# Performance work log

Hardware: AMD Instinct MI355X
Metric: run time of the kernel (lower is better)

## Reference

```python
import jax, jax.numpy as jnp
import numpy as np

B, QS, KS, E, H = 2, 2048, 2048, 2048, 16
D = E // H  # head_dim = 128
EPS = 1e-6


def setup_inputs() -> dict:
    key = jax.random.key(0)
    ks = jax.random.split(key, 11)
    scale_in = 1.0 / np.sqrt(E)  # lecun_normal fan_in = E
    scale_out = 1.0 / np.sqrt(E)  # fan_in for out proj = H*D = E
    return {
        "q": jax.random.normal(ks[0], (B, QS, E), jnp.float32),
        "kv": jax.random.normal(ks[1], (B, KS, E), jnp.float32),
        "q_pos": jax.random.normal(ks[2], (B, QS, E), jnp.float32),
        "kv_pos": jax.random.normal(ks[3], (B, KS, E), jnp.float32),
        "mask": jax.random.bernoulli(ks[4], 0.5, (B, QS, KS)),
        "wq": jax.random.normal(ks[5], (E, H, D), jnp.float32) * scale_in,
        "wk": jax.random.normal(ks[6], (E, H, D), jnp.float32) * scale_in,
        "wv": jax.random.normal(ks[7], (E, H, D), jnp.float32) * scale_in,
        "q_ln_scale": jnp.ones((D,), jnp.float32),
        "k_ln_scale": jnp.ones((D,), jnp.float32),
        "wo": jax.random.normal(ks[8], (H, D, E), jnp.float32) * scale_out,
    }


def _layernorm_no_bias(x, scale):
    # flax LayerNorm over last axis, use_bias=False, epsilon=1e-6
    mu = jnp.mean(x, axis=-1, keepdims=True)
    var = jnp.mean(jnp.square(x - mu), axis=-1, keepdims=True)
    return (x - mu) * jax.lax.rsqrt(var + EPS) * scale


def reference(q, kv, q_pos, kv_pos, mask, wq, wk, wv, q_ln_scale, k_ln_scale, wo):
    dtype = q.dtype
    qi = q + q_pos          # [b, qs, e]
    ki = kv + kv_pos        # [b, ks, e]
    vi = kv
    # QKV projections (DenseGeneral, no bias) -> [b, s, h, d]
    qh = jnp.einsum('bqe,ehd->bqhd', qi, wq)
    kh = jnp.einsum('bke,ehd->bkhd', ki, wk)
    vh = jnp.einsum('bke,ehd->bkhd', vi, wv)
    # normalize_qk: LayerNorm (no bias) on query/key over head_dim
    qh = _layernorm_no_bias(qh, q_ln_scale)
    kh = _layernorm_no_bias(kh, k_ln_scale)
    # scaled dot-product with float32 logits
    qh = qh / jnp.sqrt(jnp.asarray(D, dtype))
    logits = jnp.einsum('bqhd,bkhd->bhqk', qh, kh,
                        preferred_element_type=jnp.float32)
    big_neg = jnp.finfo(jnp.float32).min
    logits = jnp.where(mask[:, None, :, :], logits, big_neg)
    attn = jax.nn.softmax(logits, axis=-1).astype(dtype)  # [b,h,q,k]
    out = jnp.einsum('bhqk,bkhd->bqhd', attn, vh)
    # output projection (DenseGeneral over (h,d), no bias)
    return jnp.einsum('bqhd,hde->bqe', out, wo)
```

## Files before the change

### kernel.cpp

```cpp
#include <hip/hip_runtime.h>
#include <hip/hip_bf16.h>


typedef __attribute__((ext_vector_type(8))) __bf16 bf16x8;
typedef __attribute__((ext_vector_type(4))) float f32x4;
typedef __attribute__((ext_vector_type(16))) float f32x16;
typedef __attribute__((ext_vector_type(8))) unsigned short ushort8;
typedef __attribute__((ext_vector_type(4))) unsigned short ushort4v;
typedef __attribute__((ext_vector_type(4))) unsigned uint4v;
typedef __attribute__((ext_vector_type(4))) float float4v;

#define MFMA16(a, b, c) __builtin_amdgcn_mfma_f32_16x16x32_bf16((a), (b), (c), 0, 0, 0)
#define MFMA32(a, b, c) __builtin_amdgcn_mfma_f32_32x32x16_bf16((a), (b), (c), 0, 0, 0)

__device__ __forceinline__ unsigned short f2bf(float f) {
  unsigned u = __builtin_bit_cast(unsigned, f);
  u += 0x7fffu + ((u >> 16) & 1u);
  return (unsigned short)(u >> 16);
}

__device__ __forceinline__ unsigned pkbf(float lo, float hi) {
  unsigned d;
  asm("v_cvt_pk_bf16_f32 %0, %1, %2" : "=v"(d) : "v"(lo), "v"(hi));
  return d;
}

__device__ __forceinline__ float max3f(float a, float b, float c) {
  float d;
  asm("v_max3_f32 %0, %1, %2, %3" : "=v"(d) : "v"(a), "v"(b), "v"(c));
  return d;
}

__device__ __forceinline__ float exp2a(float x) {
  float d;
  asm("v_exp_f32 %0, %1" : "=v"(d) : "v"(x));
  return d;
}

__device__ __forceinline__ void gload_lds16(const void* g, void* l) {
  __builtin_amdgcn_global_load_lds(
      (const __attribute__((address_space(1))) void*)g,
      (__attribute__((address_space(3))) void*)l, 16, 0, 0);
}

__global__ __launch_bounds__(256) void k_prep(const float4v* __restrict__ q,
                                              const float4v* __restrict__ q_pos,
                                              const float4v* __restrict__ kv,
                                              const float4v* __restrict__ kv_pos,
                                              const int* __restrict__ mask,
                                              ushort4v* __restrict__ a_q,
                                              ushort4v* __restrict__ a_k,
                                              ushort4v* __restrict__ a_v,
                                              unsigned long long* __restrict__ mkb) {
  int bx = blockIdx.x, tid = threadIdx.x;
  if (bx < 8192) {
    int i = bx * 256 + tid;
    float4v a = q[i] + q_pos[i];
    ushort4v r;
    r[0] = f2bf(a[0]); r[1] = f2bf(a[1]); r[2] = f2bf(a[2]); r[3] = f2bf(a[3]);
    a_q[i] = r;
  } else if (bx < 16384) {
    int i = (bx - 8192) * 256 + tid;
    float4v a = kv[i];
    float4v s = a + kv_pos[i];
    ushort4v ra, rb;
    ra[0] = f2bf(s[0]); ra[1] = f2bf(s[1]); ra[2] = f2bf(s[2]); ra[3] = f2bf(s[3]);
    rb[0] = f2bf(a[0]); rb[1] = f2bf(a[1]); rb[2] = f2bf(a[2]); rb[3] = f2bf(a[3]);
    a_k[i] = ra; a_v[i] = rb;
  } else {
    int i = (bx - 16384) * 256 + tid;
    unsigned long long b = __ballot(mask[i] != 0);
    if ((tid & 63) == 0) mkb[i >> 6] = b;
  }
}

__global__ __launch_bounds__(256) void k_tr(const float* __restrict__ s0, const float* __restrict__ s1,
                                            const float* __restrict__ s2, const float* __restrict__ s3,
                                            unsigned short* __restrict__ d0, unsigned short* __restrict__ d1,
                                            unsigned short* __restrict__ d2, unsigned short* __restrict__ d3) {
  __shared__ float t[32][33];
  const float* S; unsigned short* D;
  switch (blockIdx.z) {
    case 0: S = s0; D = d0; break;
    case 1: S = s1; D = d1; break;
    case 2: S = s2; D = d2; break;
    default: S = s3; D = d3; break;
  }
  int x = threadIdx.x & 31, y = threadIdx.x >> 5;
  int r0 = blockIdx.y * 32, c0 = blockIdx.x * 32;
#pragma unroll
  for (int i = 0; i < 4; ++i) t[y + 8 * i][x] = S[(size_t)(r0 + y + 8 * i) * 2048 + c0 + x];
  __syncthreads();
#pragma unroll
  for (int i = 0; i < 4; ++i)
    D[(size_t)(c0 + y + 8 * i) * 2048 + r0 + x] = f2bf(t[x][y + 8 * i]);
}

template <int MODE>
__global__ __launch_bounds__(512, 2) void k_gemm8(const unsigned short* __restrict__ A,
                                                  const unsigned short* __restrict__ Bt,
                                                  void* __restrict__ Cv,
                                                  const float* __restrict__ lnsc) {
  constexpr int K = 2048;
  constexpr int NT = 32;
  constexpr int BUF = 49152;
  __shared__ __attribute__((aligned(16))) char smem[3 * BUF];
  int tid = threadIdx.x;
  int lane = tid & 63, w = tid >> 6;
  int wr = w >> 2, wc = w & 3;
  int r15 = lane & 15, blk = lane >> 4;
  int L = blockIdx.y * gridDim.x + blockIdx.x;
  int xcd = L & 7, slot = L >> 3;
  int mt, nt;
  if constexpr (MODE == 4) { mt = xcd; nt = slot; }
  else { mt = xcd * 2 + (slot >> 4); nt = slot & 15; }
  int n0 = nt * 128, m0 = mt * 256;
  const unsigned short* Abase = A + (size_t)m0 * K;
  const unsigned short* Bbase = Bt + (size_t)n0 * K;
  f32x4 acc[8][2] = {};

  const unsigned short* ag[4]; int al[4];
  const unsigned short* bg[2]; int bl[2];
#pragma unroll
  for (int i = 0; i < 4; ++i) {
    int c = i * 512 + tid;
    int row = c >> 3, cc = c & 7;
    ag[i] = Abase + (size_t)row * K + ((cc ^ (row & 7)) * 8);
    al[i] = c * 16;
  }
#pragma unroll
  for (int i = 0; i < 2; ++i) {
    int c = i * 512 + tid;
    int row = c >> 3, cc = c & 7;
    bg[i] = Bbase + (size_t)row * K + ((cc ^ (row & 7)) * 8);
    bl[i] = 32768 + c * 16;
  }

  auto stage = [&](int t) {
    char* buf = smem + (t % 3) * BUF;
    int kt = t * 64;
#pragma unroll
    for (int i = 0; i < 4; ++i) gload_lds16(ag[i] + kt, buf + al[i]);
#pragma unroll
    for (int i = 0; i < 2; ++i) gload_lds16(bg[i] + kt, buf + bl[i]);
  };

  stage(0);
  stage(1);

  for (int t = 0; t < NT; ++t) {
    if (t + 2 < NT) {
      stage(t + 2);
      asm volatile("s_waitcnt vmcnt(6)" ::: "memory");
    } else {
      asm volatile("s_waitcnt vmcnt(0)" ::: "memory");
    }
    __builtin_amdgcn_s_barrier();
    __builtin_amdgcn_sched_barrier(0);
    const unsigned short* sA = (const unsigned short*)(smem + (t % 3) * BUF);
    const unsigned short* sB = (const unsigned short*)(smem + (t % 3) * BUF + 32768);
#pragma unroll
    for (int kk = 0; kk < 2; ++kk) {
      bf16x8 av[8], bv[2];
#pragma unroll
      for (int i = 0; i < 8; ++i) {
        int row = wr * 128 + i * 16 + r15;
        av[i] = *(const bf16x8*)&sA[row * 64 + (((kk * 4 + blk) ^ (row & 7)) * 8)];
      }
#pragma unroll
      for (int j = 0; j < 2; ++j) {
        int row = wc * 32 + j * 16 + r15;
        bv[j] = *(const bf16x8*)&sB[row * 64 + (((kk * 4 + blk) ^ (row & 7)) * 8)];
      }
#pragma unroll
      for (int i = 0; i < 8; ++i)
#pragma unroll
        for (int j = 0; j < 2; ++j) acc[i][j] = MFMA16(av[i], bv[j], acc[i][j]);
    }
    asm volatile("s_waitcnt lgkmcnt(0)" ::: "memory");
    __builtin_amdgcn_s_barrier();
  }
  __syncthreads();

  if constexpr (MODE == 3) {
    float* C = (float*)Cv;
#pragma unroll
    for (int i = 0; i < 8; ++i)
#pragma unroll
      for (int r = 0; r < 4; ++r) {
        int rowl = wr * 128 + i * 16 + blk * 4 + r;
#pragma unroll
        for (int j = 0; j < 2; ++j) {
          int coll = wc * 32 + j * 16 + r15;
          C[(size_t)(m0 + rowl) * 2048 + n0 + coll] = acc[i][j][r];
        }
      }
  } else if constexpr (MODE == 4) {
    unsigned short* Vtp = (unsigned short*)Cv;
    int p15 = (r15 & 3) | ((r15 & 4) << 1) | ((r15 & 8) >> 1);
#pragma unroll
    for (int i = 0; i < 8; ++i)
#pragma unroll
      for (int r = 0; r < 4; ++r) {
        int rowg = m0 + wr * 128 + i * 16 + blk * 4 + r;
        int h = rowg >> 7, d = rowg & 127;
#pragma unroll
        for (int j = 0; j < 2; ++j) {
          int col = n0 + wc * 32 + j * 16;
          int b = col >> 11, s16 = col & 2047;
          Vtp[(((size_t)(b * 16 + h) * 128 + d) * 2048) + s16 + p15] = f2bf(acc[i][j][r]);
        }
      }
  } else {
    float* sSum = (float*)smem;
    float* sSq  = (float*)smem + 1024;
#pragma unroll
    for (int i = 0; i < 8; ++i)
#pragma unroll
      for (int r = 0; r < 4; ++r) {
        float v0 = acc[i][0][r], v1 = acc[i][1][r];
        float sm = v0 + v1, sq = v0 * v0 + v1 * v1;
        sm += __shfl_xor(sm, 1); sq += __shfl_xor(sq, 1);
        sm += __shfl_xor(sm, 2); sq += __shfl_xor(sq, 2);
        sm += __shfl_xor(sm, 4); sq += __shfl_xor(sq, 4);
        sm += __shfl_xor(sm, 8); sq += __shfl_xor(sq, 8);
        if (r15 == 0) {
          int rowl = wr * 128 + i * 16 + blk * 4 + r;
          sSum[wc * 256 + rowl] = sm;
          sSq[wc * 256 + rowl] = sq;
        }
      }
    __syncthreads();
    unsigned short* Hout = (unsigned short*)Cv;
    int h = nt;
#pragma unroll
    for (int i = 0; i < 8; ++i)
#pragma unroll
      for (int r = 0; r < 4; ++r) {
        int rowl = wr * 128 + i * 16 + blk * 4 + r;
        float sm = (sSum[rowl] + sSum[256 + rowl]) + (sSum[512 + rowl] + sSum[768 + rowl]);
        float sq = (sSq[rowl] + sSq[256 + rowl]) + (sSq[512 + rowl] + sSq[768 + rowl]);
        float mean = sm * 0.0078125f;
        float var = sq * 0.0078125f - mean * mean;
        float rstd = rsqrtf(var + 1e-6f);
        int rowg = m0 + rowl;
        int b = rowg >> 11, s = rowg & 2047;
        unsigned short* orow = Hout + (((size_t)b * 16 + h) * 2048 + s) * 128;
#pragma unroll
        for (int j = 0; j < 2; ++j) {
          int d = wc * 32 + j * 16 + r15;
          float v = acc[i][j][r];
          if constexpr (MODE == 1)
            v = (v - mean) * rstd * lnsc[d] * (0.08838834764831845f * 1.4426950408889634f);
          else
            v = (v - mean) * rstd * lnsc[d];
          orow[d] = f2bf(v);
        }
      }
  }
}

__global__ __launch_bounds__(256, 2) void k_attn(const unsigned short* __restrict__ Qh,
                                                 const unsigned short* __restrict__ Kh,
                                                 const unsigned short* __restrict__ Vtp,
                                                 const unsigned* __restrict__ maskb,
                                                 unsigned short* __restrict__ O) {
  __shared__ __attribute__((aligned(16))) char smem[65536];
  int tid = threadIdx.x, w = tid >> 6;
  int lane = tid & 63;
  int q31 = lane & 31, hi = lane >> 5;
  int L = blockIdx.y * 16 + blockIdx.x;
  int xcd = L & 7, slot = L >> 3;
  int bh = xcd * 4 + (slot >> 4);
  int qb = (slot & 15) * 128;
  int b = bh >> 4, h = bh & 15;
  size_t base = (size_t)bh * (2048 * 128);
  int qrow = qb + w * 32 + q31;

  bf16x8 qf[8];
  {
    const unsigned short* qp = Qh + base + (size_t)qrow * 128 + hi * 8;
#pragma unroll
    for (int wd = 0; wd < 8; ++wd) qf[wd] = *(const bf16x8*)(qp + wd * 16);
  }
  const unsigned* mrow = maskb + ((size_t)b * 2048 + qrow) * 64;

  const unsigned short* kgp[4];
  const unsigned short* vgp[4];
#pragma unroll
  for (int i = 0; i < 4; ++i) {
    int c = i * 256 + tid;
    int rr = c >> 4, cc = c & 15;
    kgp[i] = Kh + base + (size_t)rr * 128 + ((cc ^ (rr & 15)) * 8);
    int d = c >> 3, c8 = c & 7;
    vgp[i] = Vtp + base + (size_t)d * 2048 + ((c8 ^ (d & 7)) * 8);
  }

  f32x16 o[4] = {};
  float mv = -1e30f, ls = 0.f;

#pragma unroll
  for (int i = 0; i < 4; ++i) {
    int c = i * 256 + tid;
    gload_lds16(kgp[i], smem + c * 16);
    gload_lds16(vgp[i], smem + 16384 + c * 16);
  }
  __syncthreads();

  int cur = 0;
  for (int kc = 0; kc < 2048; kc += 64) {
    if (kc + 64 < 2048) {
      char* nb = smem + ((cur ^ 1) << 15);
#pragma unroll
      for (int i = 0; i < 4; ++i) {
        int c = i * 256 + tid;
        gload_lds16(kgp[i] + (size_t)(kc + 64) * 128, nb + c * 16);
        gload_lds16(vgp[i] + (kc + 64), nb + 16384 + c * 16);
      }
    }
    const unsigned short* sK = (const unsigned short*)(smem + (cur << 15));
    const unsigned short* sV = (const unsigned short*)(smem + (cur << 15) + 16384);

    unsigned mw0 = mrow[kc >> 5] >> (4 * hi);
    unsigned mw1 = mrow[(kc >> 5) + 1] >> (4 * hi);

    f32x16 st0 = {}, st1 = {};
    __builtin_amdgcn_s_setprio(1);
#pragma unroll
    for (int wd = 0; wd < 8; ++wd) {
      int ck = ((2 * wd + hi) ^ (q31 & 15)) * 8;
      bf16x8 k0 = *(const bf16x8*)&sK[q31 * 128 + ck];
      bf16x8 k1 = *(const bf16x8*)&sK[(32 + q31) * 128 + ck];
      st0 = MFMA32(k0, qf[wd], st0);
      st1 = MFMA32(k1, qf[wd], st1);
    }
    __builtin_amdgcn_s_setprio(0);

    float pvv[32];
#pragma unroll
    for (int r = 0; r < 16; ++r) {
      int bit = (r & 3) + 8 * (r >> 2);
      pvv[r] = ((mw0 >> bit) & 1u) ? st0[r] : -1e30f;
      pvv[16 + r] = ((mw1 >> bit) & 1u) ? st1[r] : -1e30f;
    }
    float c0 = max3f(pvv[0], pvv[1], pvv[2]);
    float c1 = max3f(pvv[3], pvv[4], pvv[5]);
    float c2 = max3f(pvv[6], pvv[7], pvv[8]);
    float c3 = max3f(pvv[9], pvv[10], pvv[11]);
    float c4 = max3f(pvv[12], pvv[13], pvv[14]);
    float c5 = max3f(pvv[15], pvv[16], pvv[17]);
    float c6 = max3f(pvv[18], pvv[19], pvv[20]);
    float c7 = max3f(pvv[21], pvv[22], pvv[23]);
    float c8 = max3f(pvv[24], pvv[25], pvv[26]);
    float c9 = max3f(pvv[27], pvv[28], pvv[29]);
    float ca = fmaxf(pvv[30], pvv[31]);
    float t0 = max3f(c0, c1, c2);
    float t1 = max3f(c3, c4, c5);
    float t2 = max3f(c6, c7, c8);
    float t3 = max3f(c9, ca, t0);
    float cmax = max3f(t1, t2, t3);
    cmax = fmaxf(cmax, __shfl_xor(cmax, 32));

    if (!__all(cmax - mv <= 11.5f)) {
      float mnew = fmaxf(mv, cmax);
      float fac = exp2a(mv - mnew);
      ls *= fac;
      float fr[16];
#pragma unroll
      for (int r = 0; r < 16; ++r) fr[r] = __shfl(fac, (r & 3) + 8 * (r >> 2) + 4 * hi);
#pragma unroll
      for (int dt = 0; dt < 4; ++dt)
#pragma unroll
        for (int r = 0; r < 16; ++r) o[dt][r] *= fr[r];
      mv = mnew;
    }

#pragma unroll
    for (int t = 0; t < 32; ++t) pvv[t] = exp2a(pvv[t] - mv);
    {
      float s0 = 0.f, s1 = 0.f, s2 = 0.f, s3 = 0.f;
#pragma unroll
      for (int t = 0; t < 8; ++t) {
        s0 += pvv[t]; s1 += pvv[8 + t]; s2 += pvv[16 + t]; s3 += pvv[24 + t];
      }
      ls += (s0 + s1) + (s2 + s3);
    }

    bf16x8 pa[4];
#pragma unroll
    for (int kw = 0; kw < 4; ++kw) {
      uint4v pw;
#pragma unroll
      for (int m = 0; m < 4; ++m) pw[m] = pkbf(pvv[8 * kw + 2 * m], pvv[8 * kw + 2 * m + 1]);
      pa[kw] = __builtin_bit_cast(bf16x8, pw);
    }

    __builtin_amdgcn_s_setprio(1);
#pragma unroll
    for (int dt = 0; dt < 4; ++dt) {
      int vrow = dt * 32 + q31;
#pragma unroll
      for (int kw = 0; kw < 4; ++kw) {
        int cv = ((2 * kw + hi) ^ (q31 & 7)) * 8;
        bf16x8 vf = *(const bf16x8*)&sV[vrow * 64 + cv];
        o[dt] = MFMA32(pa[kw], vf, o[dt]);
      }
    }
    __builtin_amdgcn_s_setprio(0);
    __syncthreads();
    cur ^= 1;
  }

  ls += __shfl_xor(ls, 32);
  float inv = 1.f / ls;
  float ir[16];
#pragma unroll
  for (int r = 0; r < 16; ++r) ir[r] = __shfl(inv, (r & 3) + 8 * (r >> 2) + 4 * hi);

  float* sO = (float*)smem;
#pragma unroll
  for (int pass = 0; pass < 2; ++pass) {
    __syncthreads();
    if ((w >> 1) == pass) {
      int wl = w & 1;
#pragma unroll
      for (int dt = 0; dt < 4; ++dt)
#pragma unroll
        for (int r = 0; r < 16; ++r) {
          int qrl = wl * 32 + (r & 3) + 8 * (r >> 2) + 4 * hi;
          sO[qrl * 132 + dt * 32 + q31] = o[dt][r] * ir[r];
        }
    }
    __syncthreads();
    {
      int row = tid >> 2, d0 = (tid & 3) * 32;
      int grow = qb + pass * 64 + row;
      unsigned short* op = O + (size_t)(b * 2048 + grow) * 2048 + h * 128 + d0;
#pragma unroll
      for (int g = 0; g < 4; ++g) {
        ushort8 pk;
#pragma unroll
        for (int e = 0; e < 8; ++e) pk[e] = f2bf(sO[row * 132 + d0 + g * 8 + e]);
        *(ushort8*)(op + g * 8) = pk;
      }
    }
  }
}

extern "C" void kernel_launch(void* const* d_in, const int* in_sizes, int n_in,
                              void* d_out, int out_size, void* d_ws, size_t ws_size,
                              hipStream_t stream) {
  const float* q      = (const float*)d_in[0];
  const float* kv     = (const float*)d_in[1];
  const float* q_pos  = (const float*)d_in[2];
  const float* kv_pos = (const float*)d_in[3];
  const int*   mask   = (const int*)d_in[4];
  const float* wq     = (const float*)d_in[5];
  const float* wk     = (const float*)d_in[6];
  const float* wv     = (const float*)d_in[7];
  const float* qls    = (const float*)d_in[8];
  const float* kls    = (const float*)d_in[9];
  const float* wo     = (const float*)d_in[10];

  char* ws = (char*)d_ws;
  const size_t SZ_ACT = (size_t)4096 * 2048 * 2;
  const size_t SZ_W   = (size_t)2048 * 2048 * 2;
  unsigned short* a_q = (unsigned short*)(ws);
  unsigned short* a_k = (unsigned short*)(ws + SZ_ACT);
  unsigned short* a_v = (unsigned short*)(ws + 2 * SZ_ACT);
  unsigned short* Qh  = (unsigned short*)(ws + 3 * SZ_ACT);
  unsigned short* Kh  = (unsigned short*)(ws + 4 * SZ_ACT);
  unsigned short* wqt = (unsigned short*)(ws + 6 * SZ_ACT);
  unsigned short* wkt = (unsigned short*)(ws + 6 * SZ_ACT + SZ_W);
  unsigned short* wvt = (unsigned short*)(ws + 6 * SZ_ACT + 2 * SZ_W);
  unsigned short* wot = (unsigned short*)(ws + 6 * SZ_ACT + 3 * SZ_W);
  unsigned*       mkb = (unsigned*)(ws + 6 * SZ_ACT + 4 * SZ_W);
  unsigned short* Ob  = a_q;
  unsigned short* Vtr = (unsigned short*)(ws + 5 * SZ_ACT);

  const size_t NEED = 6 * SZ_ACT + 4 * SZ_W + (size_t)2 * 2048 * 64 * 4;
  if (ws_size < NEED) return;

  k_prep<<<49152, 256, 0, stream>>>((const float4v*)q, (const float4v*)q_pos,
                                    (const float4v*)kv, (const float4v*)kv_pos, mask,
                                    (ushort4v*)a_q, (ushort4v*)a_k, (ushort4v*)a_v,
                                    (unsigned long long*)mkb);
  k_tr<<<dim3(64, 64, 4), 256, 0, stream>>>(wq, wk, wv, wo, wqt, wkt, wvt, wot);

  k_gemm8<1><<<dim3(16, 16), 512, 0, stream>>>(a_q, wqt, Qh, qls);
  k_gemm8<2><<<dim3(16, 16), 512, 0, stream>>>(a_k, wkt, Kh, kls);
  k_gemm8<4><<<dim3(32, 8), 512, 0, stream>>>(wvt, a_v, Vtr, nullptr);

  k_attn<<<dim3(16, 32), 256, 0, stream>>>(Qh, Kh, Vtr, mkb, Ob);

  k_gemm8<3><<<dim3(16, 16), 512, 0, stream>>>(Ob, wot, d_out, nullptr);
}
```

Baseline: 316.2 us.

## Retile projection GEMMs to 128x256 tiles with 4 waves per block

Replaces the 512-thread 256x128 GEMM with a 256-thread kernel computing 128x256 tiles. Each wave now owns a 128x64 sub-tile (8x4 MFMA accumulators), and the block-to-tile mapping is changed, including removal of the XCD-aware swizzle. The goal is fewer LDS reads per MFMA and less A-tile reloading. In exchange it raises register pressure, halves the waves per block, and changes L2 locality across XCDs.

```diff
diff --git a/kernel.cpp b/kernel.cpp
--- a/kernel.cpp
+++ b/kernel.cpp
@@ -97,43 +97,41 @@
 }
 
 template <int MODE>
-__global__ __launch_bounds__(512, 2) void k_gemm8(const unsigned short* __restrict__ A,
-                                                  const unsigned short* __restrict__ Bt,
-                                                  void* __restrict__ Cv,
-                                                  const float* __restrict__ lnsc) {
+__global__ __launch_bounds__(256) void k_gemm4(const unsigned short* __restrict__ A,
+                                               const unsigned short* __restrict__ Bt,
+                                               void* __restrict__ Cv,
+                                               const float* __restrict__ lnsc) {
   constexpr int K = 2048;
   constexpr int NT = 32;
   constexpr int BUF = 49152;
   __shared__ __attribute__((aligned(16))) char smem[3 * BUF];
   int tid = threadIdx.x;
   int lane = tid & 63, w = tid >> 6;
-  int wr = w >> 2, wc = w & 3;
   int r15 = lane & 15, blk = lane >> 4;
   int L = blockIdx.y * gridDim.x + blockIdx.x;
-  int xcd = L & 7, slot = L >> 3;
   int mt, nt;
-  if constexpr (MODE == 4) { mt = xcd; nt = slot; }
-  else { mt = xcd * 2 + (slot >> 4); nt = slot & 15; }
-  int n0 = nt * 128, m0 = mt * 256;
+  if constexpr (MODE == 4) { nt = (L & 7) + 8 * ((L >> 3) & 1); mt = L >> 4; }
+  else { nt = L & 7; mt = L >> 3; }
+  int n0 = nt * 256, m0 = mt * 128;
   const unsigned short* Abase = A + (size_t)m0 * K;
   const unsigned short* Bbase = Bt + (size_t)n0 * K;
-  f32x4 acc[8][2] = {};
+  f32x4 acc[8][4] = {};
 
   const unsigned short* ag[4]; int al[4];
-  const unsigned short* bg[2]; int bl[2];
+  const unsigned short* bg[8]; int bl[8];
 #pragma unroll
   for (int i = 0; i < 4; ++i) {
-    int c = i * 512 + tid;
+    int c = i * 256 + tid;
     int row = c >> 3, cc = c & 7;
     ag[i] = Abase + (size_t)row * K + ((cc ^ (row & 7)) * 8);
     al[i] = c * 16;
   }
 #pragma unroll
-  for (int i = 0; i < 2; ++i) {
-    int c = i * 512 + tid;
+  for (int i = 0; i < 8; ++i) {
+    int c = i * 256 + tid;
     int row = c >> 3, cc = c & 7;
     bg[i] = Bbase + (size_t)row * K + ((cc ^ (row & 7)) * 8);
-    bl[i] = 32768 + c * 16;
+    bl[i] = c * 16;
   }
 
   auto stage = [&](int t) {
@@ -142,7 +140,7 @@
 #pragma unroll
     for (int i = 0; i < 4; ++i) gload_lds16(ag[i] + kt, buf + al[i]);
 #pragma unroll
-    for (int i = 0; i < 2; ++i) gload_lds16(bg[i] + kt, buf + bl[i]);
+    for (int i = 0; i < 8; ++i) gload_lds16(bg[i] + kt, buf + 16384 + bl[i]);
   };
 
   stage(0);
@@ -151,31 +149,33 @@
   for (int t = 0; t < NT; ++t) {
     if (t + 2 < NT) {
       stage(t + 2);
-      asm volatile("s_waitcnt vmcnt(6)" ::: "memory");
+      asm volatile("s_waitcnt vmcnt(24)" ::: "memory");
+    } else if (t + 1 < NT) {
+      asm volatile("s_waitcnt vmcnt(12)" ::: "memory");
     } else {
       asm volatile("s_waitcnt vmcnt(0)" ::: "memory");
     }
     __builtin_amdgcn_s_barrier();
     __builtin_amdgcn_sched_barrier(0);
     const unsigned short* sA = (const unsigned short*)(smem + (t % 3) * BUF);
-    const unsigned short* sB = (const unsigned short*)(smem + (t % 3) * BUF + 32768);
+    const unsigned short* sB = (const unsigned short*)(smem + (t % 3) * BUF + 16384);
 #pragma unroll
     for (int kk = 0; kk < 2; ++kk) {
-      bf16x8 av[8], bv[2];
+      bf16x8 av[8], bv[4];
 #pragma unroll
       for (int i = 0; i < 8; ++i) {
-        int row = wr * 128 + i * 16 + r15;
+        int row = i * 16 + r15;
         av[i] = *(const bf16x8*)&sA[row * 64 + (((kk * 4 + blk) ^ (row & 7)) * 8)];
       }
 #pragma unroll
-      for (int j = 0; j < 2; ++j) {
-        int row = wc * 32 + j * 16 + r15;
+      for (int j = 0; j < 4; ++j) {
+        int row = w * 64 + j * 16 + r15;
         bv[j] = *(const bf16x8*)&sB[row * 64 + (((kk * 4 + blk) ^ (row & 7)) * 8)];
       }
 #pragma unroll
       for (int i = 0; i < 8; ++i)
 #pragma unroll
-        for (int j = 0; j < 2; ++j) acc[i][j] = MFMA16(av[i], bv[j], acc[i][j]);
+        for (int j = 0; j < 4; ++j) acc[i][j] = MFMA16(av[i], bv[j], acc[i][j]);
     }
     asm volatile("s_waitcnt lgkmcnt(0)" ::: "memory");
     __builtin_amdgcn_s_barrier();
@@ -188,10 +188,10 @@
     for (int i = 0; i < 8; ++i)
 #pragma unroll
       for (int r = 0; r < 4; ++r) {
-        int rowl = wr * 128 + i * 16 + blk * 4 + r;
-#pragma unroll
-        for (int j = 0; j < 2; ++j) {
-          int coll = wc * 32 + j * 16 + r15;
+        int rowl = i * 16 + blk * 4 + r;
+#pragma unroll
+        for (int j = 0; j < 4; ++j) {
+          int coll = w * 64 + j * 16 + r15;
           C[(size_t)(m0 + rowl) * 2048 + n0 + coll] = acc[i][j][r];
         }
       }
@@ -202,44 +202,46 @@
     for (int i = 0; i < 8; ++i)
 #pragma unroll
       for (int r = 0; r < 4; ++r) {
-        int rowg = m0 + wr * 128 + i * 16 + blk * 4 + r;
+        int rowg = m0 + i * 16 + blk * 4 + r;
         int h = rowg >> 7, d = rowg & 127;
 #pragma unroll
-        for (int j = 0; j < 2; ++j) {
-          int col = n0 + wc * 32 + j * 16;
+        for (int j = 0; j < 4; ++j) {
+          int col = n0 + w * 64 + j * 16;
           int b = col >> 11, s16 = col & 2047;
           Vtp[(((size_t)(b * 16 + h) * 128 + d) * 2048) + s16 + p15] = f2bf(acc[i][j][r]);
         }
       }
   } else {
     float* sSum = (float*)smem;
-    float* sSq  = (float*)smem + 1024;
+    float* sSq  = (float*)smem + 512;
 #pragma unroll
     for (int i = 0; i < 8; ++i)
 #pragma unroll
       for (int r = 0; r < 4; ++r) {
-        float v0 = acc[i][0][r], v1 = acc[i][1][r];
-        float sm = v0 + v1, sq = v0 * v0 + v1 * v1;
+        float sm = 0.f, sq = 0.f;
+#pragma unroll
+        for (int j = 0; j < 4; ++j) { float v = acc[i][j][r]; sm += v; sq += v * v; }
         sm += __shfl_xor(sm, 1); sq += __shfl_xor(sq, 1);
         sm += __shfl_xor(sm, 2); sq += __shfl_xor(sq, 2);
         sm += __shfl_xor(sm, 4); sq += __shfl_xor(sq, 4);
         sm += __shfl_xor(sm, 8); sq += __shfl_xor(sq, 8);
         if (r15 == 0) {
-          int rowl = wr * 128 + i * 16 + blk * 4 + r;
-          sSum[wc * 256 + rowl] = sm;
-          sSq[wc * 256 + rowl] = sq;
+          int rowl = i * 16 + blk * 4 + r;
+          sSum[w * 128 + rowl] = sm;
+          sSq[w * 128 + rowl] = sq;
         }
       }
     __syncthreads();
     unsigned short* Hout = (unsigned short*)Cv;
-    int h = nt;
+    int hw = w >> 1;
+    int h = nt * 2 + hw;
 #pragma unroll
     for (int i = 0; i < 8; ++i)
 #pragma unroll
       for (int r = 0; r < 4; ++r) {
-        int rowl = wr * 128 + i * 16 + blk * 4 + r;
-        float sm = (sSum[rowl] + sSum[256 + rowl]) + (sSum[512 + rowl] + sSum[768 + rowl]);
-        float sq = (sSq[rowl] + sSq[256 + rowl]) + (sSq[512 + rowl] + sSq[768 + rowl]);
+        int rowl = i * 16 + blk * 4 + r;
+        float sm = sSum[hw * 256 + rowl] + sSum[hw * 256 + 128 + rowl];
+        float sq = sSq[hw * 256 + rowl] + sSq[hw * 256 + 128 + rowl];
         float mean = sm * 0.0078125f;
         float var = sq * 0.0078125f - mean * mean;
         float rstd = rsqrtf(var + 1e-6f);
@@ -247,8 +249,8 @@
         int b = rowg >> 11, s = rowg & 2047;
         unsigned short* orow = Hout + (((size_t)b * 16 + h) * 2048 + s) * 128;
 #pragma unroll
-        for (int j = 0; j < 2; ++j) {
-          int d = wc * 32 + j * 16 + r15;
+        for (int j = 0; j < 4; ++j) {
+          int d = (w & 1) * 64 + j * 16 + r15;
           float v = acc[i][j][r];
           if constexpr (MODE == 1)
             v = (v - mean) * rstd * lnsc[d] * (0.08838834764831845f * 1.4426950408889634f);
@@ -487,11 +489,11 @@
                                     (unsigned long long*)mkb);
   k_tr<<<dim3(64, 64, 4), 256, 0, stream>>>(wq, wk, wv, wo, wqt, wkt, wvt, wot);
 
-  k_gemm8<1><<<dim3(16, 16), 512, 0, stream>>>(a_q, wqt, Qh, qls);
-  k_gemm8<2><<<dim3(16, 16), 512, 0, stream>>>(a_k, wkt, Kh, kls);
-  k_gemm8<4><<<dim3(32, 8), 512, 0, stream>>>(wvt, a_v, Vtr, nullptr);
+  k_gemm4<1><<<dim3(8, 32), 256, 0, stream>>>(a_q, wqt, Qh, qls);
+  k_gemm4<2><<<dim3(8, 32), 256, 0, stream>>>(a_k, wkt, Kh, kls);
+  k_gemm4<4><<<dim3(16, 16), 256, 0, stream>>>(wvt, a_v, Vtr, nullptr);
 
   k_attn<<<dim3(16, 32), 256, 0, stream>>>(Qh, Kh, Vtr, mkb, Ob);
 
-  k_gemm8<3><<<dim3(16, 16), 512, 0, stream>>>(Ob, wot, d_out, nullptr);
-}
+  k_gemm4<3><<<dim3(8, 32), 256, 0, stream>>>(Ob, wot, d_out, nullptr);
+}
```

Result: slower. 458.4 us (+45.0%).
